# Optimization experiments

Hardware: AMD Instinct MI355X
Metric: run time of the kernel (lower is better)

## Reference

```python
import math
import jax, jax.numpy as jnp
import numpy as np

V, D, L, H, B, T = 50257, 1024, 6, 16, 4, 1024
HD = D // H  # 64


def layer_norm(x, s, b, eps=1e-5):
    m = jnp.mean(x, axis=-1, keepdims=True)
    v = jnp.var(x, axis=-1, keepdims=True)
    return (x - m) * jax.lax.rsqrt(v + eps) * s + b


def setup_inputs() -> dict:
    key = jax.random.key(0)
    ks = jax.random.split(key, 8)
    sc = 0.02
    return {
        "input_ids": jax.random.randint(ks[0], (B, T), 0, V),
        "attention_mask": jnp.ones((B, T), jnp.float32),
        "pool_mask": jax.random.uniform(ks[1], (B, T), dtype=jnp.float32),
        "embed": jax.random.normal(ks[2], (V, D), jnp.float32) * sc,
        "ln1_s": jnp.ones((L, D), jnp.float32),
        "ln1_b": jnp.zeros((L, D), jnp.float32),
        "qkv_w": jax.random.normal(ks[3], (L, D, 3 * D), jnp.float32) * sc,
        "qkv_b": jnp.zeros((L, 3 * D), jnp.float32),
        "attn_w": jax.random.normal(ks[4], (L, D, D), jnp.float32) * sc,
        "attn_b": jnp.zeros((L, D), jnp.float32),
        "ln2_s": jnp.ones((L, D), jnp.float32),
        "ln2_b": jnp.zeros((L, D), jnp.float32),
        "fc1_w": jax.random.normal(ks[5], (L, D, 4 * D), jnp.float32) * sc,
        "fc1_b": jnp.zeros((L, 4 * D), jnp.float32),
        "fc2_w": jax.random.normal(ks[6], (L, 4 * D, D), jnp.float32) * sc,
        "fc2_b": jnp.zeros((L, D), jnp.float32),
    }


def reference(input_ids, attention_mask, pool_mask, embed, ln1_s, ln1_b,
              qkv_w, qkv_b, attn_w, attn_b, ln2_s, ln2_b,
              fc1_w, fc1_b, fc2_w, fc2_b):
    h = embed[input_ids]  # [B,T,D]
    # key_mask.clamp(min=0) then log(clamp(min=1e-9)) == log(clip(mask, 1e-9))
    log_mask = jnp.log(jnp.clip(attention_mask, 1e-9))[:, None, None, :]  # [B,1,1,T]
    scale = 1.0 / math.sqrt(HD)

    def block(h, p):
        l1s, l1b, qw, qb, aw, ab, l2s, l2b, f1w, f1b, f2w, f2b = p
        x = layer_norm(h, l1s, l1b)
        qkv = jnp.einsum('btd,de->bte', x, qw) + qb          # [B,T,3D]
        qkv = qkv.reshape(B, T, H, 3 * HD).transpose(0, 2, 1, 3)  # [B,H,T,3hd]
        q, k, v = jnp.split(qkv, 3, axis=-1)
        scores = jnp.einsum('bhqd,bhkd->bhqk', q, k) * scale + log_mask
        probs = jax.nn.softmax(scores, axis=-1)
        ctx = jnp.einsum('bhqk,bhkd->bhqd', probs, v)
        ctx = ctx.transpose(0, 2, 1, 3).reshape(B, T, D)
        h = h + jnp.einsum('btd,de->bte', ctx, aw) + ab
        y = layer_norm(h, l2s, l2b)
        y = jax.nn.gelu(jnp.einsum('btd,df->btf', y, f1w) + f1b, approximate=False)
        h = h + jnp.einsum('btf,fd->btd', y, f2w) + f2b
        # NOTE: source applies post_attention_layernorm a second time at block end
        h = layer_norm(h, l2s, l2b)
        return h, None

    params = (ln1_s, ln1_b, qkv_w, qkv_b, attn_w, attn_b,
              ln2_s, ln2_b, fc1_w, fc1_b, fc2_w, fc2_b)
    h, _ = jax.lax.scan(block, h, params)

    # pool with pool_mask, then L2-normalize (F.normalize, eps=1e-12)
    m = pool_mask[..., None]
    sent = (h * m).sum(axis=1) / jnp.clip(m.sum(axis=1), 1e-6)
    return sent / jnp.clip(jnp.linalg.norm(sent, axis=-1, keepdims=True), 1e-12)
```

## Files before the change

### kernel.cpp

```cpp
#include <hip/hip_runtime.h>
#include <hip/hip_bf16.h>
#include <math.h>

#define VV 50257
#define DD 1024
#define LL 6
#define HH 16
#define BB 4
#define TT 1024
#define HD 64
#define BT (BB*TT)

typedef __attribute__((ext_vector_type(8))) short bf16x8;
typedef __attribute__((ext_vector_type(8))) _Float16 f16x8;
typedef __attribute__((ext_vector_type(4))) float f32x4;
typedef __attribute__((ext_vector_type(16))) float f32x16;

__device__ inline float b2f(unsigned short u) {
    unsigned x = ((unsigned)u) << 16;
    return __uint_as_float(x);
}
__device__ inline unsigned short f2b(float f) {
    __hip_bfloat16 h = __float2bfloat16(f);
    return *reinterpret_cast<unsigned short*>(&h);
}
__device__ inline void plswap32(unsigned &dst, unsigned &src) {
    asm("v_permlane32_swap_b32 %0, %1" : "+v"(dst), "+v"(src));
}

#define GLOAD16(g, l) __builtin_amdgcn_global_load_lds( \
    (const __attribute__((address_space(1))) void*)(g), \
    (__attribute__((address_space(3))) void*)(l), 16, 0, 0)

__device__ inline float block_sum_256(float v, float* ws) {
    #pragma unroll
    for (int o = 32; o > 0; o >>= 1) v += __shfl_down(v, o);
    const int lane = threadIdx.x & 63, wid = threadIdx.x >> 6;
    if (lane == 0) ws[wid] = v;
    __syncthreads();
    return ws[0] + ws[1] + ws[2] + ws[3];
}

__launch_bounds__(256)
__global__ void gather_ln(const int* __restrict__ ids, const float* __restrict__ emb,
                          float* __restrict__ h, unsigned short* __restrict__ xb,
                          const float* __restrict__ g, const float* __restrict__ bta) {
    __shared__ float ws1[4], ws2[4];
    const int row = blockIdx.x, tid = threadIdx.x;
    const int id = ids[row];
    const int d = tid * 4;
    float4 v = *(const float4*)(emb + (size_t)id * DD + d);
    *(float4*)(h + (size_t)row * DD + d) = v;
    float s = v.x + v.y + v.z + v.w;
    float m = block_sum_256(s, ws1) * (1.0f / 1024.0f);
    float d0 = v.x - m, d1 = v.y - m, d2 = v.z - m, d3 = v.w - m;
    float s2 = d0*d0 + d1*d1 + d2*d2 + d3*d3;
    float rstd = rsqrtf(block_sum_256(s2, ws2) * (1.0f / 1024.0f) + 1e-5f);
    float4 gg = *(const float4*)(g + d);
    float4 bb = *(const float4*)(bta + d);
    ushort4 o;
    o.x = f2b(d0 * rstd * gg.x + bb.x);
    o.y = f2b(d1 * rstd * gg.y + bb.y);
    o.z = f2b(d2 * rstd * gg.z + bb.z);
    o.w = f2b(d3 * rstd * gg.w + bb.w);
    *(ushort4*)(xb + (size_t)row * DD + d) = o;
}

__launch_bounds__(256)
__global__ void logmask_k(const float* __restrict__ am, float* __restrict__ lm) {
    int i = blockIdx.x * 256 + threadIdx.x;
    if (i < BT) lm[i] = logf(fmaxf(am[i], 1e-9f));
}

__launch_bounds__(256)
__global__ void ln_f32(const float* __restrict__ in, float* __restrict__ out,
                       const float* __restrict__ g, const float* __restrict__ bta) {
    __shared__ float ws1[4], ws2[4];
    const int row = blockIdx.x, tid = threadIdx.x;
    const float* x = in + (size_t)row * DD;
    float4 v = *(const float4*)(x + tid * 4);
    float s = v.x + v.y + v.z + v.w;
    float m = block_sum_256(s, ws1) * (1.0f / 1024.0f);
    float d0 = v.x - m, d1 = v.y - m, d2 = v.z - m, d3 = v.w - m;
    float s2 = d0*d0 + d1*d1 + d2*d2 + d3*d3;
    float rstd = rsqrtf(block_sum_256(s2, ws2) * (1.0f / 1024.0f) + 1e-5f);
    const int d = tid * 4;
    float4 gg = *(const float4*)(g + d);
    float4 bb = *(const float4*)(bta + d);
    float4 o;
    o.x = d0 * rstd * gg.x + bb.x;
    o.y = d1 * rstd * gg.y + bb.y;
    o.z = d2 * rstd * gg.z + bb.z;
    o.w = d3 * rstd * gg.w + bb.w;
    *(float4*)(out + (size_t)row * DD + d) = o;
}

__launch_bounds__(256)
__global__ void ln_bf16(const float* __restrict__ in, unsigned short* __restrict__ out,
                        const float* __restrict__ g, const float* __restrict__ bta) {
    __shared__ float ws1[4], ws2[4];
    const int row = blockIdx.x, tid = threadIdx.x;
    const float* x = in + (size_t)row * DD;
    float4 v = *(const float4*)(x + tid * 4);
    float s = v.x + v.y + v.z + v.w;
    float m = block_sum_256(s, ws1) * (1.0f / 1024.0f);
    float d0 = v.x - m, d1 = v.y - m, d2 = v.z - m, d3 = v.w - m;
    float s2 = d0*d0 + d1*d1 + d2*d2 + d3*d3;
    float rstd = rsqrtf(block_sum_256(s2, ws2) * (1.0f / 1024.0f) + 1e-5f);
    const int d = tid * 4;
    float4 gg = *(const float4*)(g + d);
    float4 bb = *(const float4*)(bta + d);
    ushort4 o;
    o.x = f2b(d0 * rstd * gg.x + bb.x);
    o.y = f2b(d1 * rstd * gg.y + bb.y);
    o.z = f2b(d2 * rstd * gg.z + bb.z);
    o.w = f2b(d3 * rstd * gg.w + bb.w);
    *(ushort4*)(out + (size_t)row * DD + d) = o;
}

__launch_bounds__(256)
__global__ void ln_dual(const float* __restrict__ in, float* __restrict__ outf,
                        const float* __restrict__ g2, const float* __restrict__ b2v,
                        unsigned short* __restrict__ outb,
                        const float* __restrict__ g1, const float* __restrict__ b1v) {
    __shared__ float ws1[4], ws2[4], ws3[4], ws4[4];
    const int row = blockIdx.x, tid = threadIdx.x;
    const int d = tid * 4;
    float4 v = *(const float4*)(in + (size_t)row * DD + d);
    float s = v.x + v.y + v.z + v.w;
    float m = block_sum_256(s, ws1) * (1.0f / 1024.0f);
    float d0 = v.x - m, d1 = v.y - m, d2 = v.z - m, d3 = v.w - m;
    float s2 = d0*d0 + d1*d1 + d2*d2 + d3*d3;
    float rstd = rsqrtf(block_sum_256(s2, ws2) * (1.0f / 1024.0f) + 1e-5f);
    float4 gg = *(const float4*)(g2 + d);
    float4 bb = *(const float4*)(b2v + d);
    float4 y;
    y.x = d0 * rstd * gg.x + bb.x;
    y.y = d1 * rstd * gg.y + bb.y;
    y.z = d2 * rstd * gg.z + bb.z;
    y.w = d3 * rstd * gg.w + bb.w;
    *(float4*)(outf + (size_t)row * DD + d) = y;
    float t = y.x + y.y + y.z + y.w;
    float m2 = block_sum_256(t, ws3) * (1.0f / 1024.0f);
    float e0 = y.x - m2, e1 = y.y - m2, e2 = y.z - m2, e3 = y.w - m2;
    float t2 = e0*e0 + e1*e1 + e2*e2 + e3*e3;
    float rstd2 = rsqrtf(block_sum_256(t2, ws4) * (1.0f / 1024.0f) + 1e-5f);
    float4 g1v = *(const float4*)(g1 + d);
    float4 b1x = *(const float4*)(b1v + d);
    ushort4 o;
    o.x = f2b(e0 * rstd2 * g1v.x + b1x.x);
    o.y = f2b(e1 * rstd2 * g1v.y + b1x.y);
    o.z = f2b(e2 * rstd2 * g1v.z + b1x.z);
    o.w = f2b(e3 * rstd2 * g1v.w + b1x.w);
    *(ushort4*)(outb + (size_t)row * DD + d) = o;
}

__launch_bounds__(256)
__global__ void wtrans_all(const float* __restrict__ wq, unsigned short* __restrict__ wqo,
                           const float* __restrict__ wa, unsigned short* __restrict__ wao,
                           const float* __restrict__ w1, unsigned short* __restrict__ w1o,
                           const float* __restrict__ w2, unsigned short* __restrict__ w2o) {
    __shared__ float tile[64][65];
    const int l = blockIdx.x / 3072;
    int id = blockIdx.x % 3072;
    const float* W; unsigned short* Wt; int K, N, tx, ty;
    if (id < 768)       { W = wq + (size_t)l*1024*3072; Wt = wqo + (size_t)l*3072*1024; K = 1024; N = 3072; tx = id % 48; ty = id / 48; }
    else if (id < 1024) { id -= 768;  W = wa + (size_t)l*1024*1024; Wt = wao + (size_t)l*1024*1024; K = 1024; N = 1024; tx = id & 15; ty = id >> 4; }
    else if (id < 2048) { id -= 1024; W = w1 + (size_t)l*1024*4096; Wt = w1o + (size_t)l*4096*1024; K = 1024; N = 4096; tx = id & 63; ty = id >> 6; }
    else                { id -= 2048; W = w2 + (size_t)l*4096*1024; Wt = w2o + (size_t)l*1024*4096; K = 4096; N = 1024; tx = id & 15; ty = id >> 4; }
    const int k0 = ty * 64, n0 = tx * 64;
    const int lrow = threadIdx.x >> 4;
    const int lcol = (threadIdx.x & 15) * 4;
    #pragma unroll
    for (int i = 0; i < 4; ++i) {
        const int r = lrow + i * 16;
        *(float4*)&tile[r][lcol] = *(const float4*)(W + (size_t)(k0 + r) * N + n0 + lcol);
    }
    __syncthreads();
    #pragma unroll
    for (int i = 0; i < 4; ++i) {
        const int n = lrow + i * 16;
        ushort4 o;
        o.x = f2b(tile[lcol + 0][n]);
        o.y = f2b(tile[lcol + 1][n]);
        o.z = f2b(tile[lcol + 2][n]);
        o.w = f2b(tile[lcol + 3][n]);
        *(ushort4*)(Wt + (size_t)(n0 + n) * K + k0 + lcol) = o;
    }
}

#define BM 128
#define BK 64

__device__ inline float gelu_f(float v) {
    return 0.5f * v * (1.0f + erff(v * 0.70710678118654752f));
}

template<int EPI, int NF32>
__launch_bounds__(256)
__global__ void gemm_mfma(const unsigned short* __restrict__ A,
                          const unsigned short* __restrict__ Bt,
                          const float* __restrict__ bias, void* __restrict__ Cv,
                          int M, int K, int N) {
    constexpr int BN = NF32 * 64;
    __shared__ short As[BM * BK];
    __shared__ short Bs[BN * BK];

    const int tid = threadIdx.x;
    const int wid = tid >> 6, lane = tid & 63;
    const int lo = lane & 31, hf = lane >> 5;

    const int nwg = gridDim.x * gridDim.y;
    int bid = blockIdx.y * gridDim.x + blockIdx.x;
    bid = (bid & 7) * (nwg >> 3) + (bid >> 3);
    const int m0 = (bid / gridDim.x) * BM;
    const int n0 = (bid % gridDim.x) * BN;

    const int wr = wid >> 1, wc = wid & 1;

    const int rowS = tid >> 3, cS = tid & 7;
    const int coff = (cS ^ (rowS & 7)) * 8;
    const unsigned short* aS = A  + (size_t)(m0 + rowS) * K + coff;
    const unsigned short* bS = Bt + (size_t)(n0 + rowS) * K + coff;
    const size_t rstride = (size_t)32 * K;

    int cph[4];
    #pragma unroll
    for (int ks = 0; ks < 4; ++ks) cph[ks] = ((ks * 2 + hf) ^ (lo & 7)) * 8;
    int arow[2], brow[NF32];
    #pragma unroll
    for (int m = 0; m < 2; ++m) arow[m] = (wr * 64 + m * 32 + lo) * BK;
    #pragma unroll
    for (int n = 0; n < NF32; ++n) brow[n] = (wc * NF32 * 32 + n * 32 + lo) * BK;

    f32x16 acc[2][NF32];
    #pragma unroll
    for (int m = 0; m < 2; ++m)
        #pragma unroll
        for (int n = 0; n < NF32; ++n)
            #pragma unroll
            for (int j = 0; j < 16; ++j) acc[m][n][j] = 0.f;

    for (int kk = 0; kk < K; kk += BK) {
        __syncthreads();
        #pragma unroll
        for (int r = 0; r < 4; ++r)
            GLOAD16(aS + kk + r * rstride, &As[(wid * 64 + r * 256) * 8]);
        #pragma unroll
        for (int r = 0; r < 2 * NF32; ++r)
            GLOAD16(bS + kk + r * rstride, &Bs[(wid * 64 + r * 256) * 8]);
        __syncthreads();
        #pragma unroll
        for (int ks = 0; ks < 4; ++ks) {
            bf16x8 af[2], bfr[NF32];
            #pragma unroll
            for (int m = 0; m < 2; ++m) af[m] = *(const bf16x8*)&As[arow[m] + cph[ks]];
            #pragma unroll
            for (int n = 0; n < NF32; ++n) bfr[n] = *(const bf16x8*)&Bs[brow[n] + cph[ks]];
            #pragma unroll
            for (int m = 0; m < 2; ++m)
                #pragma unroll
                for (int n = 0; n < NF32; ++n)
                    acc[m][n] = __builtin_amdgcn_mfma_f32_32x32x16_bf16(
                        af[m], bfr[n], acc[m][n], 0, 0, 0);
        }
    }

    #pragma unroll
    for (int n = 0; n < NF32; ++n) {
        const int col = n0 + wc * NF32 * 32 + n * 32 + lo;
        const float bias_v = bias[col];
        #pragma unroll
        for (int m = 0; m < 2; ++m) {
            const int rbase = m0 + wr * 64 + m * 32 + 4 * hf;
            #pragma unroll
            for (int j = 0; j < 16; ++j) {
                const int row = rbase + (j & 3) + 8 * (j >> 2);
                float v = acc[m][n][j] + bias_v;
                if (EPI == 1) {
                    float* C = (float*)Cv;
                    C[(size_t)row * N + col] += v;
                } else {
                    if (EPI == 2) v = gelu_f(v);
                    unsigned short* C = (unsigned short*)Cv;
                    C[(size_t)row * N + col] = f2b(v);
                }
            }
        }
    }
}

__launch_bounds__(256)
__global__ void attn_mfma(const unsigned short* __restrict__ qkv,
                          const float* __restrict__ lm,
                          unsigned short* __restrict__ ctx) {
    int bid = blockIdx.x;
    const int ww = (bid & 7) * 64 + (bid >> 3);
    const int bh = ww >> 3, qt = ww & 7;
    const int b = bh >> 4, hh = bh & 15;
    const int tid = threadIdx.x, w = tid >> 6, lane = tid & 63;
    const int lo = lane & 31, hf = lane >> 5;
    const int q_row = qt * 128 + w * 32 + lo;

    __shared__ short Ks[2][64 * 64];
    __shared__ short Vt[2][64 * 72];
    __shared__ float lms[2][64];

    bf16x8 qf[4];
    {
        const unsigned short* qbase = qkv + (size_t)(b * TT + q_row) * 3072 + hh * 192;
        #pragma unroll
        for (int kk = 0; kk < 4; ++kk)
            qf[kk] = *(const bf16x8*)(qbase + (2 * kk + hf) * 8);
    }

    const int r0 = tid >> 3, cS = tid & 7;
    const unsigned short* kp = qkv + (size_t)(b * TT + r0) * 3072 + hh * 192 + 64
                               + ((cS ^ (r0 & 7)) * 8);
    const int vkey = tid & 31, vc = tid >> 5;
    const unsigned short* vp = qkv + (size_t)(b * TT + vkey) * 3072 + hh * 192 + 128 + vc * 8;
    const float* lmrow = lm + b * TT;

    f32x16 o0, o1;
    #pragma unroll
    for (int j = 0; j < 16; ++j) { o0[j] = 0.f; o1[j] = 0.f; }
    float M = -1e30f, S = 0.f;

    {
        GLOAD16(kp, &Ks[0][(w * 64) * 8]);
        GLOAD16(kp + (size_t)32 * 3072, &Ks[0][(256 + w * 64) * 8]);
        bf16x8 v0 = *(const bf16x8*)vp;
        bf16x8 v1 = *(const bf16x8*)(vp + (size_t)32 * 3072);
        if (tid < 64) lms[0][tid] = lmrow[tid];
        #pragma unroll
        for (int i = 0; i < 8; ++i) {
            _Float16 h0 = (_Float16)b2f((unsigned short)v0[i]);
            _Float16 h1 = (_Float16)b2f((unsigned short)v1[i]);
            Vt[0][(vc * 8 + i) * 72 + vkey] = *reinterpret_cast<short*>(&h0);
            Vt[0][(vc * 8 + i) * 72 + 32 + vkey] = *reinterpret_cast<short*>(&h1);
        }
    }

    int cur = 0;
    for (int kt = 0; kt < 16; ++kt) {
        __syncthreads();
        if (kt < 15) {
            const int nb = cur ^ 1;
            const size_t off = (size_t)((kt + 1) * 64) * 3072;
            GLOAD16(kp + off, &Ks[nb][(w * 64) * 8]);
            GLOAD16(kp + off + (size_t)32 * 3072, &Ks[nb][(256 + w * 64) * 8]);
            bf16x8 v0 = *(const bf16x8*)(vp + off);
            bf16x8 v1 = *(const bf16x8*)(vp + off + (size_t)32 * 3072);
            if (tid < 64) lms[nb][tid] = lmrow[(kt + 1) * 64 + tid];
            #pragma unroll
            for (int i = 0; i < 8; ++i) {
                _Float16 h0 = (_Float16)b2f((unsigned short)v0[i]);
                _Float16 h1 = (_Float16)b2f((unsigned short)v1[i]);
                Vt[nb][(vc * 8 + i) * 72 + vkey] = *reinterpret_cast<short*>(&h0);
                Vt[nb][(vc * 8 + i) * 72 + 32 + vkey] = *reinterpret_cast<short*>(&h1);
            }
        }

        #pragma unroll
        for (int g = 0; g < 2; ++g) {
            f32x16 s16;
            #pragma unroll
            for (int j = 0; j < 16; ++j) s16[j] = 0.f;
            __builtin_amdgcn_s_setprio(1);
            #pragma unroll
            for (int kk = 0; kk < 4; ++kk) {
                const int c = (2 * kk + hf) ^ (lo & 7);
                bf16x8 kf = *(const bf16x8*)&Ks[cur][((g * 32 + lo) * 8 + c) * 8];
                s16 = __builtin_amdgcn_mfma_f32_32x32x16_bf16(kf, qf[kk], s16, 0, 0, 0);
            }
            __builtin_amdgcn_s_setprio(0);

            float p[16];
            float mx = -1e30f;
            #pragma unroll
            for (int j = 0; j < 16; ++j) {
                const int kidx = g * 32 + (j & 3) + 8 * (j >> 2) + 4 * hf;
                float sv = s16[j] * 0.125f + lms[cur][kidx];
                p[j] = sv;
                mx = fmaxf(mx, sv);
            }
            mx = fmaxf(mx, __shfl_xor(mx, 32));
            if (!__all(mx <= M + 8.0f)) {
                const float Mn = fmaxf(M, mx);
                const float f = __expf(M - Mn);
                S *= f;
                #pragma unroll
                for (int j = 0; j < 16; ++j) { o0[j] *= f; o1[j] *= f; }
                M = Mn;
            }

            unsigned short ph[16];
            float ls = 0.f;
            #pragma unroll
            for (int j = 0; j < 16; ++j) {
                _Float16 hq = (_Float16)__expf(p[j] - M);
                ph[j] = *reinterpret_cast<unsigned short*>(&hq);
                ls += (float)hq;
            }
            ls += __shfl_xor(ls, 32);
            S += ls;

            unsigned ra = (unsigned)ph[0]  | ((unsigned)ph[1]  << 16);
            unsigned rb = (unsigned)ph[2]  | ((unsigned)ph[3]  << 16);
            unsigned rc = (unsigned)ph[4]  | ((unsigned)ph[5]  << 16);
            unsigned rd = (unsigned)ph[6]  | ((unsigned)ph[7]  << 16);
            unsigned re = (unsigned)ph[8]  | ((unsigned)ph[9]  << 16);
            unsigned rf = (unsigned)ph[10] | ((unsigned)ph[11] << 16);
            unsigned rg = (unsigned)ph[12] | ((unsigned)ph[13] << 16);
            unsigned rh = (unsigned)ph[14] | ((unsigned)ph[15] << 16);
            plswap32(ra, rc);
            plswap32(rb, rd);
            plswap32(re, rg);
            plswap32(rf, rh);
            union { unsigned u[4]; f16x8 v; } p1, p2;
            p1.u[0] = ra; p1.u[1] = rb; p1.u[2] = rc; p1.u[3] = rd;
            p2.u[0] = re; p2.u[1] = rf; p2.u[2] = rg; p2.u[3] = rh;

            f16x8 va0 = *(const f16x8*)&Vt[cur][lo * 72 + g * 32 + hf * 8];
            f16x8 va1 = *(const f16x8*)&Vt[cur][lo * 72 + g * 32 + 16 + hf * 8];
            f16x8 vb0 = *(const f16x8*)&Vt[cur][(32 + lo) * 72 + g * 32 + hf * 8];
            f16x8 vb1 = *(const f16x8*)&Vt[cur][(32 + lo) * 72 + g * 32 + 16 + hf * 8];
            __builtin_amdgcn_s_setprio(1);
            o0 = __builtin_amdgcn_mfma_f32_32x32x16_f16(va0, p1.v, o0, 0, 0, 0);
            o0 = __builtin_amdgcn_mfma_f32_32x32x16_f16(va1, p2.v, o0, 0, 0, 0);
            o1 = __builtin_amdgcn_mfma_f32_32x32x16_f16(vb0, p1.v, o1, 0, 0, 0);
            o1 = __builtin_amdgcn_mfma_f32_32x32x16_f16(vb1, p2.v, o1, 0, 0, 0);
            __builtin_amdgcn_s_setprio(0);
        }
        cur ^= 1;
    }

    const float inv = 1.f / S;
    unsigned short* obase = ctx + (size_t)(b * TT + q_row) * DD + hh * 64;
    #pragma unroll
    for (int g = 0; g < 4; ++g) {
        const int dbase = 8 * g + 4 * hf;
        ushort4 w0, w1;
        w0.x = f2b(o0[4*g+0] * inv); w0.y = f2b(o0[4*g+1] * inv);
        w0.z = f2b(o0[4*g+2] * inv); w0.w = f2b(o0[4*g+3] * inv);
        w1.x = f2b(o1[4*g+0] * inv); w1.y = f2b(o1[4*g+1] * inv);
        w1.z = f2b(o1[4*g+2] * inv); w1.w = f2b(o1[4*g+3] * inv);
        *(ushort4*)(obase + dbase) = w0;
        *(ushort4*)(obase + 32 + dbase) = w1;
    }
}

__launch_bounds__(256)
__global__ void pool_partial(const float* __restrict__ h, const float* __restrict__ pm,
                             float* __restrict__ part) {
    const int b = blockIdx.x >> 4, c = blockIdx.x & 15;
    const int tid = threadIdx.x;
    const float* hp = h + (size_t)(b * TT + c * 64) * DD + tid * 4;
    const float* pp = pm + b * TT + c * 64;
    float4 acc = {0.f, 0.f, 0.f, 0.f};
    for (int t = 0; t < 64; ++t) {
        const float p = pp[t];
        float4 v = *(const float4*)(hp + (size_t)t * DD);
        acc.x += p * v.x; acc.y += p * v.y; acc.z += p * v.z; acc.w += p * v.w;
    }
    *(float4*)(part + (size_t)blockIdx.x * DD + tid * 4) = acc;
}

__launch_bounds__(1024)
__global__ void pool_final(const float* __restrict__ part, const float* __restrict__ pm,
                           float* __restrict__ out) {
    const int b = blockIdx.x, d = threadIdx.x;
    __shared__ float ws[16];
    float s = pm[b * TT + d];
    #pragma unroll
    for (int o = 32; o > 0; o >>= 1) s += __shfl_down(s, o);
    if ((d & 63) == 0) ws[d >> 6] = s;
    __syncthreads();
    float msum = 0.f;
    #pragma unroll
    for (int i = 0; i < 16; ++i) msum += ws[i];

    float acc = 0.f;
    #pragma unroll
    for (int c = 0; c < 16; ++c)
        acc += part[(size_t)(b * 16 + c) * DD + d];
    const float sent = acc / fmaxf(msum, 1e-6f);

    float qv = sent * sent;
    #pragma unroll
    for (int o = 32; o > 0; o >>= 1) qv += __shfl_down(qv, o);
    __syncthreads();
    if ((d & 63) == 0) ws[d >> 6] = qv;
    __syncthreads();
    float nrm = 0.f;
    #pragma unroll
    for (int i = 0; i < 16; ++i) nrm += ws[i];
    nrm = sqrtf(nrm);
    out[b * DD + d] = sent / fmaxf(nrm, 1e-12f);
}

extern "C" void kernel_launch(void* const* d_in, const int* in_sizes, int n_in,
                              void* d_out, int out_size, void* d_ws, size_t ws_size,
                              hipStream_t stream) {
    const int*   ids    = (const int*)  d_in[0];
    const float* amask  = (const float*)d_in[1];
    const float* pmask  = (const float*)d_in[2];
    const float* embed  = (const float*)d_in[3];
    const float* ln1_s  = (const float*)d_in[4];
    const float* ln1_b  = (const float*)d_in[5];
    const float* qkv_w  = (const float*)d_in[6];
    const float* qkv_b  = (const float*)d_in[7];
    const float* attn_w = (const float*)d_in[8];
    const float* attn_b = (const float*)d_in[9];
    const float* ln2_s  = (const float*)d_in[10];
    const float* ln2_b  = (const float*)d_in[11];
    const float* fc1_w  = (const float*)d_in[12];
    const float* fc1_b  = (const float*)d_in[13];
    const float* fc2_w  = (const float*)d_in[14];
    const float* fc2_b  = (const float*)d_in[15];

    char* wp = (char*)d_ws;
    float* h = (float*)wp;                 wp += (size_t)BT * DD * 4;
    unsigned short* qkv_bf = (unsigned short*)wp; wp += (size_t)BT * 3072 * 2;
    unsigned short* act_bf = (unsigned short*)wp; wp += (size_t)BT * 4096 * 2;
    unsigned short* x_bf   = (unsigned short*)wp; wp += (size_t)BT * DD * 2;
    unsigned short* wq_t   = (unsigned short*)wp; wp += (size_t)LL * 3072 * 1024 * 2;
    unsigned short* wa_t   = (unsigned short*)wp; wp += (size_t)LL * 1024 * 1024 * 2;
    unsigned short* w1_t   = (unsigned short*)wp; wp += (size_t)LL * 4096 * 1024 * 2;
    unsigned short* w2_t   = (unsigned short*)wp; wp += (size_t)LL * 1024 * 4096 * 2;
    float* lm = (float*)wp;                wp += (size_t)BT * 4;
    float* part = (float*)wp;              wp += (size_t)64 * DD * 4;

    gather_ln<<<BT, 256, 0, stream>>>(ids, embed, h, x_bf, ln1_s, ln1_b);
    logmask_k<<<16, 256, 0, stream>>>(amask, lm);
    wtrans_all<<<LL * 3072, 256, 0, stream>>>(qkv_w, wq_t, attn_w, wa_t,
                                              fc1_w, w1_t, fc2_w, w2_t);

    for (int l = 0; l < LL; ++l) {
        const size_t lD = (size_t)l * DD;
        const unsigned short* wq = wq_t + (size_t)l * 3072 * 1024;
        const unsigned short* wa = wa_t + (size_t)l * 1024 * 1024;
        const unsigned short* w1 = w1_t + (size_t)l * 4096 * 1024;
        const unsigned short* w2 = w2_t + (size_t)l * 1024 * 4096;

        gemm_mfma<0, 2><<<dim3(3072/128, BT/BM), 256, 0, stream>>>(
            x_bf, wq, qkv_b + (size_t)l * 3072, qkv_bf, BT, 1024, 3072);
        attn_mfma<<<512, 256, 0, stream>>>(qkv_bf, lm, x_bf);
        gemm_mfma<1, 1><<<dim3(1024/64, BT/BM), 256, 0, stream>>>(
            x_bf, wa, attn_b + lD, h, BT, 1024, 1024);
        ln_bf16<<<BT, 256, 0, stream>>>(h, x_bf, ln2_s + lD, ln2_b + lD);
        gemm_mfma<2, 2><<<dim3(4096/128, BT/BM), 256, 0, stream>>>(
            x_bf, w1, fc1_b + (size_t)l * 4096, act_bf, BT, 1024, 4096);
        gemm_mfma<1, 1><<<dim3(1024/64, BT/BM), 256, 0, stream>>>(
            act_bf, w2, fc2_b + lD, h, BT, 4096, 1024);

        if (l < LL - 1) {
            ln_dual<<<BT, 256, 0, stream>>>(h, h, ln2_s + lD, ln2_b + lD,
                                            x_bf, ln1_s + lD + DD, ln1_b + lD + DD);
        } else {
            ln_f32<<<BT, 256, 0, stream>>>(h, h, ln2_s + lD, ln2_b + lD);
        }
    }

    pool_partial<<<64, 256, 0, stream>>>(h, pmask, part);
    pool_final<<<BB, 1024, 0, stream>>>(part, pmask, (float*)d_out);
}
```

Before: 1.808 ms.

## Double-buffer GEMM LDS tiles and switch to 16x16x32 MFMA with BK=32

Rewrites the GEMM main loop to double-buffer shared-memory tiles, issuing the next K-tile's global-to-LDS loads before computing on the current one, which removes one barrier per iteration. BK drops from 64 to 32 and the MFMA shape changes from 32x32x16 to 16x16x32, with new swizzle and fragment indexing and a revised epilogue. The aim is to overlap memory loads with MFMA work. The trade-off is twice as many loop iterations with less compute per barrier, and smaller MFMA tiles that need more LDS reads per FLOP.

```diff
diff --git a/kernel.cpp b/kernel.cpp
--- a/kernel.cpp
+++ b/kernel.cpp
@@ -190,25 +190,25 @@
 }
 
 #define BM 128
-#define BK 64
+#define BK 32
 
 __device__ inline float gelu_f(float v) {
     return 0.5f * v * (1.0f + erff(v * 0.70710678118654752f));
 }
 
-template<int EPI, int NF32>
+template<int EPI, int NFRAG>
 __launch_bounds__(256)
 __global__ void gemm_mfma(const unsigned short* __restrict__ A,
                           const unsigned short* __restrict__ Bt,
                           const float* __restrict__ bias, void* __restrict__ Cv,
                           int M, int K, int N) {
-    constexpr int BN = NF32 * 64;
-    __shared__ short As[BM * BK];
-    __shared__ short Bs[BN * BK];
+    constexpr int BN = NFRAG * 32;
+    constexpr int BG = NFRAG / 2;
+    __shared__ short As[2][BM * BK];
+    __shared__ short Bs[2][BN * BK];
 
     const int tid = threadIdx.x;
     const int wid = tid >> 6, lane = tid & 63;
-    const int lo = lane & 31, hf = lane >> 5;
 
     const int nwg = gridDim.x * gridDim.y;
     int bid = blockIdx.y * gridDim.x + blockIdx.x;
@@ -217,66 +217,74 @@
     const int n0 = (bid % gridDim.x) * BN;
 
     const int wr = wid >> 1, wc = wid & 1;
-
-    const int rowS = tid >> 3, cS = tid & 7;
-    const int coff = (cS ^ (rowS & 7)) * 8;
-    const unsigned short* aS = A  + (size_t)(m0 + rowS) * K + coff;
-    const unsigned short* bS = Bt + (size_t)(n0 + rowS) * K + coff;
-    const size_t rstride = (size_t)32 * K;
-
-    int cph[4];
-    #pragma unroll
-    for (int ks = 0; ks < 4; ++ks) cph[ks] = ((ks * 2 + hf) ^ (lo & 7)) * 8;
-    int arow[2], brow[NF32];
-    #pragma unroll
-    for (int m = 0; m < 2; ++m) arow[m] = (wr * 64 + m * 32 + lo) * BK;
-    #pragma unroll
-    for (int n = 0; n < NF32; ++n) brow[n] = (wc * NF32 * 32 + n * 32 + lo) * BK;
-
-    f32x16 acc[2][NF32];
-    #pragma unroll
-    for (int m = 0; m < 2; ++m)
-        #pragma unroll
-        for (int n = 0; n < NF32; ++n)
-            #pragma unroll
-            for (int j = 0; j < 16; ++j) acc[m][n][j] = 0.f;
-
-    for (int kk = 0; kk < K; kk += BK) {
+    const int fr = lane & 15, fq = lane >> 4;
+
+    const int rowS = tid >> 2;
+    const int blkS = tid & 3;
+    const int swz0 = (rowS >> 1) & 3;
+    const unsigned short* aS0 = A  + (size_t)(m0 + rowS)      * K + (blkS ^ swz0) * 8;
+    const unsigned short* aS1 = A  + (size_t)(m0 + rowS + 64) * K + (blkS ^ swz0) * 8;
+    const unsigned short* bS0 = Bt + (size_t)(n0 + rowS)      * K + (blkS ^ swz0) * 8;
+    const unsigned short* bS1 = Bt + (size_t)(n0 + rowS + 64) * K + (blkS ^ swz0) * 8;
+
+    const int sF = (fr >> 1) & 3;
+    int aoff[4], boff[NFRAG];
+    #pragma unroll
+    for (int m = 0; m < 4; ++m) aoff[m] = (wr * 64 + m * 16 + fr) * BK + ((fq ^ sF) * 8);
+    #pragma unroll
+    for (int n = 0; n < NFRAG; ++n) boff[n] = (wc * (NFRAG * 16) + n * 16 + fr) * BK + ((fq ^ sF) * 8);
+
+    f32x4 acc[4][NFRAG];
+    #pragma unroll
+    for (int m = 0; m < 4; ++m)
+        #pragma unroll
+        for (int n = 0; n < NFRAG; ++n) acc[m][n] = (f32x4){0.f, 0.f, 0.f, 0.f};
+
+    const int T = K / BK;
+
+    GLOAD16(aS0, &As[0][(wid * 64) * 8]);
+    GLOAD16(aS1, &As[0][(256 + wid * 64) * 8]);
+    GLOAD16(bS0, &Bs[0][(wid * 64) * 8]);
+    if (BG > 1) GLOAD16(bS1, &Bs[0][(256 + wid * 64) * 8]);
+
+    int cur = 0;
+    for (int t = 0; t < T; ++t) {
         __syncthreads();
-        #pragma unroll
-        for (int r = 0; r < 4; ++r)
-            GLOAD16(aS + kk + r * rstride, &As[(wid * 64 + r * 256) * 8]);
-        #pragma unroll
-        for (int r = 0; r < 2 * NF32; ++r)
-            GLOAD16(bS + kk + r * rstride, &Bs[(wid * 64 + r * 256) * 8]);
-        __syncthreads();
-        #pragma unroll
-        for (int ks = 0; ks < 4; ++ks) {
-            bf16x8 af[2], bfr[NF32];
-            #pragma unroll
-            for (int m = 0; m < 2; ++m) af[m] = *(const bf16x8*)&As[arow[m] + cph[ks]];
-            #pragma unroll
-            for (int n = 0; n < NF32; ++n) bfr[n] = *(const bf16x8*)&Bs[brow[n] + cph[ks]];
-            #pragma unroll
-            for (int m = 0; m < 2; ++m)
-                #pragma unroll
-                for (int n = 0; n < NF32; ++n)
-                    acc[m][n] = __builtin_amdgcn_mfma_f32_32x32x16_bf16(
-                        af[m], bfr[n], acc[m][n], 0, 0, 0);
+        if (t + 1 < T) {
+            const int nb = cur ^ 1;
+            const size_t ko = (size_t)(t + 1) * BK;
+            GLOAD16(aS0 + ko, &As[nb][(wid * 64) * 8]);
+            GLOAD16(aS1 + ko, &As[nb][(256 + wid * 64) * 8]);
+            GLOAD16(bS0 + ko, &Bs[nb][(wid * 64) * 8]);
+            if (BG > 1) GLOAD16(bS1 + ko, &Bs[nb][(256 + wid * 64) * 8]);
         }
-    }
-
-    #pragma unroll
-    for (int n = 0; n < NF32; ++n) {
-        const int col = n0 + wc * NF32 * 32 + n * 32 + lo;
-        const float bias_v = bias[col];
-        #pragma unroll
-        for (int m = 0; m < 2; ++m) {
-            const int rbase = m0 + wr * 64 + m * 32 + 4 * hf;
-            #pragma unroll
-            for (int j = 0; j < 16; ++j) {
-                const int row = rbase + (j & 3) + 8 * (j >> 2);
-                float v = acc[m][n][j] + bias_v;
+        bf16x8 af[4], bfr[NFRAG];
+        #pragma unroll
+        for (int m = 0; m < 4; ++m) af[m] = *(const bf16x8*)&As[cur][aoff[m]];
+        #pragma unroll
+        for (int n = 0; n < NFRAG; ++n) bfr[n] = *(const bf16x8*)&Bs[cur][boff[n]];
+        #pragma unroll
+        for (int m = 0; m < 4; ++m)
+            #pragma unroll
+            for (int n = 0; n < NFRAG; ++n)
+                acc[m][n] = __builtin_amdgcn_mfma_f32_16x16x32_bf16(
+                    af[m], bfr[n], acc[m][n], 0, 0, 0);
+        cur ^= 1;
+    }
+
+    float bias_v[NFRAG];
+    #pragma unroll
+    for (int n = 0; n < NFRAG; ++n) bias_v[n] = bias[n0 + wc * (NFRAG * 16) + n * 16 + fr];
+
+    #pragma unroll
+    for (int m = 0; m < 4; ++m) {
+        #pragma unroll
+        for (int n = 0; n < NFRAG; ++n) {
+            const int col = n0 + wc * (NFRAG * 16) + n * 16 + fr;
+            #pragma unroll
+            for (int j = 0; j < 4; ++j) {
+                const int row = m0 + wr * 64 + m * 16 + fq * 4 + j;
+                float v = acc[m][n][j] + bias_v[n];
                 if (EPI == 1) {
                     float* C = (float*)Cv;
                     C[(size_t)row * N + col] += v;
@@ -543,15 +551,15 @@
         const unsigned short* w1 = w1_t + (size_t)l * 4096 * 1024;
         const unsigned short* w2 = w2_t + (size_t)l * 1024 * 4096;
 
-        gemm_mfma<0, 2><<<dim3(3072/128, BT/BM), 256, 0, stream>>>(
+        gemm_mfma<0, 4><<<dim3(3072/128, BT/BM), 256, 0, stream>>>(
             x_bf, wq, qkv_b + (size_t)l * 3072, qkv_bf, BT, 1024, 3072);
         attn_mfma<<<512, 256, 0, stream>>>(qkv_bf, lm, x_bf);
-        gemm_mfma<1, 1><<<dim3(1024/64, BT/BM), 256, 0, stream>>>(
+        gemm_mfma<1, 2><<<dim3(1024/64, BT/BM), 256, 0, stream>>>(
             x_bf, wa, attn_b + lD, h, BT, 1024, 1024);
         ln_bf16<<<BT, 256, 0, stream>>>(h, x_bf, ln2_s + lD, ln2_b + lD);
-        gemm_mfma<2, 2><<<dim3(4096/128, BT/BM), 256, 0, stream>>>(
+        gemm_mfma<2, 4><<<dim3(4096/128, BT/BM), 256, 0, stream>>>(
             x_bf, w1, fc1_b + (size_t)l * 4096, act_bf, BT, 1024, 4096);
-        gemm_mfma<1, 1><<<dim3(1024/64, BT/BM), 256, 0, stream>>>(
+        gemm_mfma<1, 2><<<dim3(1024/64, BT/BM), 256, 0, stream>>>(
             act_bf, w2, fc2_b + lD, h, BT, 4096, 1024);
 
         if (l < LL - 1) {
```

Measured after the change: 1.751 ms. 3.2% less time.
